# Optimization experiments

Measured on AMD Instinct MI355X. Metric: run time of the kernel, lower is better.

Reference implementation:

```python
import jax, jax.numpy as jnp
import numpy as np

B, C_IN, C_OUT = 32, 64, 128
K_SIZE, STRIDE, PAD, H = 3, 1, 1, 56
H_OUT = (H + 2 * PAD - K_SIZE) // STRIDE + 1


def setup_inputs() -> dict:
    key = jax.random.key(0)
    kx, kw = jax.random.split(key)
    x = jax.random.normal(kx, (B, C_IN, H, H), dtype=jnp.float32)
    # kaiming_uniform-ish init for K of shape [kh, kw, C_in, C_out]
    fan_in = K_SIZE * C_IN * C_OUT  # torch fan_in for this layout (dim1 * receptive field)
    bound = np.sqrt(6.0 / fan_in).astype(np.float32)
    K = jax.random.uniform(kw, (K_SIZE, K_SIZE, C_IN, C_OUT), dtype=jnp.float32,
                           minval=-bound, maxval=bound)
    return {"x": x, "K": K}


def reference(x, K):
    # Faithful to the torch code INCLUDING its mismatched flatten orders:
    #   patch flattened as (C_in, kh, kw); K flattened as (kh, kw, C_in).
    xp = jnp.pad(x, ((0, 0), (0, 0), (PAD, PAD), (PAD, PAD)))
    end = (H_OUT - 1) * STRIDE + 1
    # patches[b, c, di, dj, i, j] = xp[b, c, i*stride+di, j*stride+dj]
    rows = []
    for di in range(K_SIZE):
        cols = []
        for dj in range(K_SIZE):
            cols.append(xp[:, :, di:di + end:STRIDE, dj:dj + end:STRIDE])  # [B,C,Ho,Wo]
        rows.append(jnp.stack(cols, axis=2))  # [B,C,kw,Ho,Wo]
    patches = jnp.stack(rows, axis=2)  # [B, C, kh, kw, Ho, Wo]
    # flatten patch in (C, kh, kw) order -> [B, Ho, Wo, C*kh*kw]
    p = patches.transpose(0, 4, 5, 1, 2, 3).reshape(B, H_OUT, H_OUT, -1)
    # K flattened in (kh, kw, C) order, exactly as K.view(-1, out_channels)
    Kf = K.reshape(-1, C_OUT)  # [kh*kw*C_in, C_out]
    out = p @ Kf  # [B, Ho, Wo, C_out]
    return out.transpose(0, 3, 1, 2)  # [B, C_out, Ho, Wo]
```

## Files before the change

### kernel.cpp

```cpp
#include <hip/hip_runtime.h>
#include <hip/hip_bf16.h>
#include <stdint.h>


#define B_   32
#define CIN  64
#define COUT 128
#define H_   56
#define HP   58
#define F_   576

typedef __attribute__((ext_vector_type(8))) short bf16x8;
typedef __attribute__((ext_vector_type(4))) float f32x4;

#define XP_ELEMS (B_*HP*HP*CIN)
#define XP_SLACK 4096
#define XP_TOTAL (XP_ELEMS + XP_SLACK)
#define WG_ELEMS (COUT*F_)
#define WS_NEEDED ((size_t)(XP_TOTAL + WG_ELEMS) * 2)

#define NROW   (B_*HP)
#define NWBLK  (WG_ELEMS/256)

#define A_ALLOC 32768
#define LDS_TOT (A_ALLOC + 2*8192)

__global__ __launch_bounds__(256) void prep_all(const float* __restrict__ x,
                                                const float* __restrict__ K,
                                                __hip_bfloat16* __restrict__ xpT,
                                                __hip_bfloat16* __restrict__ WgT) {
  const int id = blockIdx.x;
  const int t  = threadIdx.x;

  if (id > NROW) {
    int n = (id - (NROW + 1))*256 + t;
    int co = n / F_, g = n % F_;
    int di = g / 192, dj = (g % 192) / 64, c = g & 63;
    int f  = c*9 + di*3 + dj;
    int kh = f / 192, kw = (f % 192) / 64, cc = f & 63;
    WgT[n] = __float2bfloat16(K[(((size_t)kh*3 + kw)*CIN + cc)*COUT + co]);
    return;
  }
  if (id == NROW) {
    bf16x8 z = (bf16x8)0;
    for (int idx = t; idx < XP_SLACK/8; idx += 256)
      ((bf16x8*)(xpT + XP_ELEMS))[idx] = z;
    return;
  }

  const int b = id / HP, h = id % HP;
  __hip_bfloat16* orow = xpT + (size_t)(b*HP + h) * HP * CIN;
  if (h == 0 || h == HP-1) {
    bf16x8 z = (bf16x8)0;
    for (int idx = t; idx < HP*CIN/8; idx += 256) ((bf16x8*)orow)[idx] = z;
    return;
  }
  __shared__ __align__(16) float scr[CIN*64];
  const float* xrow = x + ((size_t)(b*CIN)*H_ + (h-1)) * H_;
  for (int idx = t; idx < CIN*14; idx += 256) {
    int c = idx / 14, w4 = idx % 14;
    f32x4 v = *(const f32x4*)(xrow + (size_t)c*(H_*H_) + w4*4);
    *(f32x4*)&scr[c*64 + ((w4 + (c >> 3)) & 15)*4] = v;
  }
  __syncthreads();
  for (int idx = t; idx < HP*8; idx += 256) {
    int wp = idx >> 3, cg = (idx & 7) * 8;
    __align__(16) __hip_bfloat16 tmp[8];
    if (wp == 0 || wp == HP-1) {
#pragma unroll
      for (int k2 = 0; k2 < 8; ++k2) tmp[k2] = __float2bfloat16(0.f);
    } else {
      int w = wp - 1, sl = w >> 2, off = w & 3;
#pragma unroll
      for (int k2 = 0; k2 < 8; ++k2) {
        int c = cg + k2;
        tmp[k2] = __float2bfloat16(scr[c*64 + ((sl + (c >> 3)) & 15)*4 + off]);
      }
    }
    *(bf16x8*)(orow + (size_t)wp*CIN + cg) = *(const bf16x8*)tmp;
  }
}

__global__ __launch_bounds__(256, 3) void conv_mfma(
    const __hip_bfloat16* __restrict__ xpT,
    const __hip_bfloat16* __restrict__ WgT,
    float* __restrict__ out) {
  __shared__ __align__(16) char lds[LDS_TOT];
  const int t    = threadIdx.x;
  const int wave = t >> 6;
  const int l    = t & 63;
  const int lr   = l & 15, lq = l >> 4;
  const int wm   = wave >> 1, wn = wave & 1;

  const int bid = blockIdx.x;
  const int swz = (bid & 7) * 112 + (bid >> 3);
  const int bb  = swz / 28;
  const int i0  = (swz % 28) * 2;

  f32x4 acc[4][4];
#pragma unroll
  for (int mi = 0; mi < 4; ++mi)
#pragma unroll
    for (int ni = 0; ni < 4; ++ni) acc[mi][ni] = (f32x4)0.f;

  const char* xb    = (const char*)xpT + (size_t)(bb*HP + i0) * HP * CIN * 2;
  const char* wbase = (const char*)WgT;

#pragma unroll
  for (int s = 0; s < 8; ++s) {
    int o = s*4096 + t*16;
    int m = o >> 7;
    const char* src = xb + ((o & ~127) | ((o & 127) ^ ((m & 7) << 4)));
    __builtin_amdgcn_global_load_lds(
        (const __attribute__((address_space(1))) void*)src,
        (__attribute__((address_space(3))) void*)(lds + s*4096 + wave*1024),
        16, 0, 0);
  }

  int bsrc[2];
#pragma unroll
  for (int s = 0; s < 2; ++s) {
    int f  = s*256 + t;
    int ll = f & 63;
    int co = ((f >> 6)*16) + (ll & 15);
    bsrc[s] = co*1152 + ((ll >> 4)*16);
  }

  auto stageBh = [&](int hc, int buf) {
    const char* wg = wbase + hc*64;
    char* Bb = lds + A_ALLOC + buf*8192;
#pragma unroll
    for (int s = 0; s < 2; ++s) {
      __builtin_amdgcn_global_load_lds(
          (const __attribute__((address_space(1))) void*)(wg + bsrc[s]),
          (__attribute__((address_space(3))) void*)(Bb + s*4096 + wave*1024),
          16, 0, 0);
    }
  };

  stageBh(0, 0);
  __syncthreads();

#pragma unroll
  for (int hc = 0; hc < 18; ++hc) {
    const int buf = hc & 1;
    if (hc < 17) stageBh(hc + 1, buf ^ 1);
    const char* Bb = lds + A_ALLOC + buf*8192;
    const int kg  = hc*32;
    const int di  = kg / 192;
    const int rem = kg - di*192;
    bf16x8 a[4], bq[4];
#pragma unroll
    for (int mi = 0; mi < 4; ++mi) {
      int r   = (wm + di)*HP + mi*16 + lr;
      int tot = r*128 + rem*2 + lq*16;
      int adr = (tot & ~127) | ((tot & 127) ^ (((tot >> 7) & 7) << 4));
      a[mi] = *(const bf16x8*)(lds + adr);
    }
#pragma unroll
    for (int ni = 0; ni < 4; ++ni)
      bq[ni] = *(const bf16x8*)(Bb + ((wn*4 + ni)*64 + l)*16);
    __builtin_amdgcn_s_setprio(1);
#pragma unroll
    for (int mi = 0; mi < 4; ++mi)
#pragma unroll
      for (int ni = 0; ni < 4; ++ni)
        acc[mi][ni] = __builtin_amdgcn_mfma_f32_16x16x32_bf16(
            a[mi], bq[ni], acc[mi][ni], 0, 0, 0);
    __builtin_amdgcn_s_setprio(0);
    __syncthreads();
  }

  const int i = i0 + wm;
#pragma unroll
  for (int mi = 0; mi < 4; ++mi) {
    int j0 = mi*16 + lq*4;
    if (j0 < H_) {
#pragma unroll
      for (int ni = 0; ni < 4; ++ni) {
        int co = wn*64 + ni*16 + lr;
        float* dst = out + (((size_t)(bb*COUT + co))*H_ + i)*H_ + j0;
        *(f32x4*)dst = acc[mi][ni];
      }
    }
  }
}

__global__ __launch_bounds__(256) void conv_naive(const float* __restrict__ x,
                                                  const float* __restrict__ K,
                                                  float* __restrict__ out) {
  int idx = blockIdx.x*256 + threadIdx.x;
  const int total = B_*COUT*H_*H_;
  if (idx >= total) return;
  int j = idx % H_, i = (idx / H_) % H_, co = (idx / (H_*H_)) % COUT, b = idx / (H_*H_*COUT);
  float s = 0.f;
  for (int c = 0; c < CIN; ++c)
    for (int di = 0; di < 3; ++di) {
      int ii = i + di - 1;
      if (ii < 0 || ii >= H_) continue;
      for (int dj = 0; dj < 3; ++dj) {
        int jj = j + dj - 1;
        if (jj < 0 || jj >= H_) continue;
        int f = c*9 + di*3 + dj;
        int kh = f / 192, kw = (f % 192) / 64, cc = f & 63;
        s += x[(((size_t)b*CIN + c)*H_ + ii)*H_ + jj] *
             K[(((size_t)kh*3 + kw)*CIN + cc)*COUT + co];
      }
    }
  out[idx] = s;
}

extern "C" void kernel_launch(void* const* d_in, const int* in_sizes, int n_in,
                              void* d_out, int out_size, void* d_ws, size_t ws_size,
                              hipStream_t stream) {
  const float* x = (const float*)d_in[0];
  const float* K = (const float*)d_in[1];
  float* out = (float*)d_out;
  if (ws_size >= WS_NEEDED) {
    __hip_bfloat16* xpT = (__hip_bfloat16*)d_ws;
    __hip_bfloat16* WgT = xpT + XP_TOTAL;
    prep_all<<<NROW + 1 + NWBLK, 256, 0, stream>>>(x, K, xpT, WgT);
    conv_mfma<<<B_*28, 256, 0, stream>>>(xpT, WgT, out);
  } else {
    conv_naive<<<(B_*COUT*H_*H_ + 255)/256, 256, 0, stream>>>(x, K, out);
  }
}
```

Baseline: 45.30 us.

## Load weight fragments directly into registers instead of staging through LDS

Weight (B) fragments are now read straight from global memory into registers and double-buffered across K-steps, where before they were staged into LDS. This removes the per-iteration __syncthreads and the B LDS buffers, shrinking shared memory from 48KB to 32KB, which may allow higher occupancy. In exchange it adds register pressure and direct global-to-register loads whose latency must be hidden by the register prefetch. The weights are small and shared by all blocks, so they should mostly hit in cache.

```diff
diff --git a/kernel.cpp b/kernel.cpp
--- a/kernel.cpp
+++ b/kernel.cpp
@@ -21,9 +21,6 @@
 
 #define NROW   (B_*HP)
 #define NWBLK  (WG_ELEMS/256)
-
-#define A_ALLOC 32768
-#define LDS_TOT (A_ALLOC + 2*8192)
 
 __global__ __launch_bounds__(256) void prep_all(const float* __restrict__ x,
                                                 const float* __restrict__ K,
@@ -85,7 +82,7 @@
     const __hip_bfloat16* __restrict__ xpT,
     const __hip_bfloat16* __restrict__ WgT,
     float* __restrict__ out) {
-  __shared__ __align__(16) char lds[LDS_TOT];
+  __shared__ __align__(16) char lds[32768];
   const int t    = threadIdx.x;
   const int wave = t >> 6;
   const int l    = t & 63;
@@ -103,8 +100,7 @@
 #pragma unroll
     for (int ni = 0; ni < 4; ++ni) acc[mi][ni] = (f32x4)0.f;
 
-  const char* xb    = (const char*)xpT + (size_t)(bb*HP + i0) * HP * CIN * 2;
-  const char* wbase = (const char*)WgT;
+  const char* xb = (const char*)xpT + (size_t)(bb*HP + i0) * HP * CIN * 2;
 
 #pragma unroll
   for (int s = 0; s < 8; ++s) {
@@ -116,40 +112,28 @@
         (__attribute__((address_space(3))) void*)(lds + s*4096 + wave*1024),
         16, 0, 0);
   }
-
-  int bsrc[2];
-#pragma unroll
-  for (int s = 0; s < 2; ++s) {
-    int f  = s*256 + t;
-    int ll = f & 63;
-    int co = ((f >> 6)*16) + (ll & 15);
-    bsrc[s] = co*1152 + ((ll >> 4)*16);
-  }
-
-  auto stageBh = [&](int hc, int buf) {
-    const char* wg = wbase + hc*64;
-    char* Bb = lds + A_ALLOC + buf*8192;
-#pragma unroll
-    for (int s = 0; s < 2; ++s) {
-      __builtin_amdgcn_global_load_lds(
-          (const __attribute__((address_space(1))) void*)(wg + bsrc[s]),
-          (__attribute__((address_space(3))) void*)(Bb + s*4096 + wave*1024),
-          16, 0, 0);
-    }
+  __syncthreads();
+
+  const char* wB = (const char*)WgT + (size_t)(wn*64 + lr)*1152 + lq*16;
+
+  auto loadB = [&](int hc, bf16x8 (&bq)[4]) {
+#pragma unroll
+    for (int ni = 0; ni < 4; ++ni)
+      bq[ni] = *(const bf16x8*)(wB + ni*(16*1152) + hc*64);
   };
 
-  stageBh(0, 0);
-  __syncthreads();
+  bf16x8 b0[4], b1[4];
+  loadB(0, b0);
 
 #pragma unroll
   for (int hc = 0; hc < 18; ++hc) {
-    const int buf = hc & 1;
-    if (hc < 17) stageBh(hc + 1, buf ^ 1);
-    const char* Bb = lds + A_ALLOC + buf*8192;
+    bf16x8 (&bc)[4] = (hc & 1) ? b1 : b0;
+    bf16x8 (&bn)[4] = (hc & 1) ? b0 : b1;
+    if (hc < 17) loadB(hc + 1, bn);
     const int kg  = hc*32;
     const int di  = kg / 192;
     const int rem = kg - di*192;
-    bf16x8 a[4], bq[4];
+    bf16x8 a[4];
 #pragma unroll
     for (int mi = 0; mi < 4; ++mi) {
       int r   = (wm + di)*HP + mi*16 + lr;
@@ -157,18 +141,14 @@
       int adr = (tot & ~127) | ((tot & 127) ^ (((tot >> 7) & 7) << 4));
       a[mi] = *(const bf16x8*)(lds + adr);
     }
-#pragma unroll
-    for (int ni = 0; ni < 4; ++ni)
-      bq[ni] = *(const bf16x8*)(Bb + ((wn*4 + ni)*64 + l)*16);
     __builtin_amdgcn_s_setprio(1);
 #pragma unroll
     for (int mi = 0; mi < 4; ++mi)
 #pragma unroll
       for (int ni = 0; ni < 4; ++ni)
         acc[mi][ni] = __builtin_amdgcn_mfma_f32_16x16x32_bf16(
-            a[mi], bq[ni], acc[mi][ni], 0, 0, 0);
+            a[mi], bc[ni], acc[mi][ni], 0, 0, 0);
     __builtin_amdgcn_s_setprio(0);
-    __syncthreads();
   }
 
   const int i = i0 + wm;
```

Result: slower. 57.81 us (+27.6%).
